# Kernel tuning notes

Measured on AMD Instinct MI355X. Metric: run time of the kernel, lower is better.

The kernel has to match this reference:

```python
import jax, jax.numpy as jnp
import numpy as np

B, C, H, W = 4, 64, 128, 128

def conv1x1(x, w, b):
    # x: [B,Ci,H,W], w: [Co,Ci], b: [Co]
    return jnp.einsum('bchw,oc->bohw', x, w) + b[None, :, None, None]

def setup_inputs() -> dict:
    key = jax.random.key(0)
    ks = jax.random.split(key, 10)
    d = {}
    d['x'] = jax.random.normal(ks[0], (B, C, H, W), dtype=jnp.float32)
    # patchmerging params: LayerNorm(4C) + Linear(4C -> C)
    d['pm_gamma'] = jnp.ones((4 * C,), jnp.float32)
    d['pm_beta'] = jnp.zeros((4 * C,), jnp.float32)
    d['pm_w'] = jax.random.normal(ks[1], (C, 4 * C), jnp.float32) * 0.02
    d['pm_b'] = jnp.zeros((C,), jnp.float32)
    # 1x1 convs: conv2..conv6 are C->C, conv1 is 2C->C
    for i, n in enumerate(['2', '3', '4', '5', '6']):
        d['w' + n] = jax.random.normal(ks[2 + i], (C, C), jnp.float32) * 0.05
        d['b' + n] = jnp.zeros((C,), jnp.float32)
    d['w1'] = jax.random.normal(ks[7], (C, 2 * C), jnp.float32) * 0.05
    d['b1'] = jnp.zeros((C,), jnp.float32)
    return d

def reference(x, pm_gamma, pm_beta, pm_w, pm_b,
              w1, b1, w2, b2, w3, b3, w4, b4, w5, b5, w6, b6):
    Bx, Cx, Hx, Wx = x.shape
    Hh, Wh = Hx // 2, Wx // 2
    N = Hh * Wh
    # ---- patch merging ----
    x0 = x[:, :, 0::2, 0::2]
    x1_ = x[:, :, 1::2, 0::2]
    x2_ = x[:, :, 0::2, 1::2]
    x3_ = x[:, :, 1::2, 1::2]
    m = jnp.concatenate([x0, x1_, x2_, x3_], axis=1)        # [B,4C,Hh,Wh]
    t = m.reshape(Bx, 4 * Cx, N).transpose(0, 2, 1)          # [B,N,4C]
    mu = t.mean(-1, keepdims=True)
    var = t.var(-1, keepdims=True)
    t = (t - mu) / jnp.sqrt(var + 1e-5) * pm_gamma + pm_beta  # LayerNorm eps=1e-5
    t = t @ pm_w.T + pm_b                                     # [B,N,C]
    c1 = t.transpose(0, 2, 1).reshape(Bx, Cx, Hh, Wh)
    # ---- spatial attention (PAM-style) ----
    q = conv1x1(c1, w2, b2).reshape(Bx, Cx, N)
    k = conv1x1(c1, w3, b3).reshape(Bx, Cx, N)
    v = conv1x1(c1, w4, b4).reshape(Bx, Cx, N)
    qk1 = jax.nn.softmax(jnp.einsum('bcn,bcm->bnm', q, k), axis=-1)  # [B,N,N]
    # torch: out1 = v @ qk1.permute(0,2,1) -> out1[b,c,j] = sum_i v[b,c,i]*qk1[b,j,i]
    out1 = jnp.einsum('bci,bji->bcj', v, qk1).reshape(Bx, Cx, Hh, Wh)
    # ---- channel attention (CAM-style) ----
    q2 = conv1x1(c1, w5, b5).reshape(Bx, Cx, N)
    k2 = conv1x1(c1, w6, b6).reshape(Bx, Cx, N)
    qk2 = jax.nn.softmax(jnp.einsum('bcn,bdn->bcd', q2, k2), axis=-1)  # [B,C,C]
    out2 = jnp.einsum('bcd,bdn->bcn', qk2, v).reshape(Bx, Cx, Hh, Wh)
    # ---- fuse, 1x1 conv, bilinear upsample x2 (align_corners=False), residual ----
    out = jnp.concatenate([out1, out2], axis=1)              # [B,2C,Hh,Wh]
    out = conv1x1(out, w1, b1)                               # [B,C,Hh,Wh]
    out = jax.image.resize(out, (Bx, Cx, Hx, Wx), method='bilinear')
    return out + x
```

## Files before the change

kernel.cpp:

```cpp
#include <hip/hip_runtime.h>

typedef __attribute__((ext_vector_type(8))) short bf16x8;
typedef __attribute__((ext_vector_type(4))) float fx4;

struct __attribute__((aligned(8))) sh4 { short x, y, z, w; };

#define OPART_B   0u
#define LSUM_B    12582912u
#define SMALL_B   12976128u
#define L2M_B     17170432u
#define C1B_B     17235968u
#define QB_B      19333120u
#define KB_B      21430272u
#define VCN_B     23527424u
#define VNC_B     25624576u
#define Q2B_B     27721728u
#define K2B_B     29818880u

static __device__ __forceinline__ short f2bf(float f) {
  unsigned u = __float_as_uint(f);
  unsigned r = (u + 0x7FFFu + ((u >> 16) & 1u)) >> 16;
  return (short)r;
}
static __device__ __forceinline__ short f2bf_fast(float f) {
  return (short)((__float_as_uint(f) + 0x8000u) >> 16);
}
static __device__ __forceinline__ float bf2f(short s) {
  return __uint_as_float(((unsigned)(unsigned short)s) << 16);
}
static __device__ __forceinline__ bf16x8 ld8f(const float* p) {
  float4 p0 = *(const float4*)p;
  float4 p1 = *(const float4*)(p + 4);
  bf16x8 r;
  r[0] = f2bf(p0.x); r[1] = f2bf(p0.y); r[2] = f2bf(p0.z); r[3] = f2bf(p0.w);
  r[4] = f2bf(p1.x); r[5] = f2bf(p1.y); r[6] = f2bf(p1.z); r[7] = f2bf(p1.w);
  return r;
}

__global__ __launch_bounds__(256) void patchln_kernel(
    const float* __restrict__ x, const float* __restrict__ gamma,
    const float* __restrict__ beta, const float* __restrict__ pm_w,
    const float* __restrict__ pm_b, short* __restrict__ c1b, float* __restrict__ l2m)
{
  __shared__ short tnb[32*264];
  __shared__ float red_s[512];
  __shared__ float mu_s[32], rs_s[32];
  const int b   = blockIdx.y;
  const int i   = blockIdx.x >> 1;
  const int jh  = blockIdx.x & 1;
  const int tid = threadIdx.x;
  const int j   = tid & 31;
  const int g8  = tid >> 5;
  const int jj  = jh*32 + j;

  if (blockIdx.x == 0) {
    #pragma unroll
    for (int k = 0; k < 16; ++k) l2m[(size_t)b*4096 + k*256 + tid] = 0.0f;
  }

  float vals[32];
  float sm = 0.f, sq = 0.f;
  #pragma unroll
  for (int k = 0; k < 16; ++k) {
    int p  = g8*16 + k;
    int cc = p & 63, di = p >> 6;
    float2 v2 = *(const float2*)&x[((size_t)(b*64 + cc)*128 + 2*i + di)*128 + 2*jj];
    vals[2*k]   = v2.x;
    vals[2*k+1] = v2.y;
    sm += v2.x + v2.y; sq += v2.x*v2.x + v2.y*v2.y;
  }
  red_s[g8*32 + j] = sm;
  red_s[256 + g8*32 + j] = sq;
  __syncthreads();
  if (tid < 32) {
    float s0 = 0.f, q0 = 0.f;
    #pragma unroll
    for (int g = 0; g < 8; ++g) { s0 += red_s[g*32 + tid]; q0 += red_s[256 + g*32 + tid]; }
    float mu  = s0 * (1.0f/256.0f);
    float var = q0 * (1.0f/256.0f) - mu*mu;
    mu_s[tid] = mu;
    rs_s[tid] = rsqrtf(var + 1e-5f);
  }
  __syncthreads();
  {
    float mu = mu_s[j], rs = rs_s[j];
    #pragma unroll
    for (int k = 0; k < 16; ++k) {
      int p  = g8*16 + k;
      int ca = p, cb = p + 128;
      tnb[j*264 + ca] = f2bf((vals[2*k]   - mu)*rs*gamma[ca] + beta[ca]);
      tnb[j*264 + cb] = f2bf((vals[2*k+1] - mu)*rs*gamma[cb] + beta[cb]);
    }
  }
  __syncthreads();

  const int w    = tid >> 6;
  const int lane = tid & 63;
  const int L15  = lane & 15;
  const int quad = lane >> 4;
  fx4 d0 = {0.f,0.f,0.f,0.f}, d1 = {0.f,0.f,0.f,0.f};
  #pragma unroll
  for (int kc = 0; kc < 8; ++kc) {
    bf16x8 a = ld8f(pm_w + (w*16 + L15)*256 + kc*32 + quad*8);
    bf16x8 bf0 = *(const bf16x8*)&tnb[(L15)*264      + kc*32 + quad*8];
    bf16x8 bf1 = *(const bf16x8*)&tnb[(16 + L15)*264 + kc*32 + quad*8];
    d0 = __builtin_amdgcn_mfma_f32_16x16x32_bf16(a, bf0, d0, 0, 0, 0);
    d1 = __builtin_amdgcn_mfma_f32_16x16x32_bf16(a, bf1, d1, 0, 0, 0);
  }
  const int obase = w*16 + quad*4;
  float bias0 = pm_b[obase], bias1 = pm_b[obase+1], bias2 = pm_b[obase+2], bias3 = pm_b[obase+3];
  const int gn0 = i*64 + jh*32 + L15;
  sh4 s0; s0.x = f2bf(d0[0]+bias0); s0.y = f2bf(d0[1]+bias1); s0.z = f2bf(d0[2]+bias2); s0.w = f2bf(d0[3]+bias3);
  sh4 s1; s1.x = f2bf(d1[0]+bias0); s1.y = f2bf(d1[1]+bias1); s1.z = f2bf(d1[2]+bias2); s1.w = f2bf(d1[3]+bias3);
  *(sh4*)&c1b[((size_t)b*4096 + gn0)*64 + obase]      = s0;
  *(sh4*)&c1b[((size_t)b*4096 + gn0 + 16)*64 + obase] = s1;
}

__global__ __launch_bounds__(256) void proj5_kernel(
    const short* __restrict__ c1b,
    const float* __restrict__ w2f, const float* __restrict__ w3f, const float* __restrict__ w4f,
    const float* __restrict__ w5f, const float* __restrict__ w6f,
    const float* __restrict__ b2, const float* __restrict__ b3, const float* __restrict__ b4,
    const float* __restrict__ b5, const float* __restrict__ b6,
    short* __restrict__ qb, short* __restrict__ kb,
    short* __restrict__ vcn, short* __restrict__ vnc,
    short* __restrict__ q2b, short* __restrict__ k2b)
{
  __shared__ short ldsT[4*16*72];
  const int b    = blockIdx.y;
  const int tid  = threadIdx.x;
  const int w    = tid >> 6;
  const int nsub = w & 1;
  const int pg   = w >> 1;
  const int lane = tid & 63;
  const int L15  = lane & 15;
  const int quad = lane >> 4;
  const int gn0  = blockIdx.x*32 + nsub*16;
  const int gn   = gn0 + L15;
  short* T = ldsT + w*16*72;

  bf16x8 bf0 = *(const bf16x8*)&c1b[((size_t)b*4096 + gn)*64 + quad*8];
  bf16x8 bf1 = *(const bf16x8*)&c1b[((size_t)b*4096 + gn)*64 + quad*8 + 32];

  if (pg == 0) {
    const float* wp[2] = {w2f, w3f};
    const float* bp[2] = {b2, b3};
    #pragma unroll
    for (int p = 0; p < 2; ++p) {
      short* dst = (p == 0) ? qb : kb;
      #pragma unroll
      for (int mt = 0; mt < 4; ++mt) {
        bf16x8 a0 = ld8f(wp[p] + (mt*16 + L15)*64 + quad*8);
        bf16x8 a1 = ld8f(wp[p] + (mt*16 + L15)*64 + quad*8 + 32);
        fx4 d = {0.f,0.f,0.f,0.f};
        d = __builtin_amdgcn_mfma_f32_16x16x32_bf16(a0, bf0, d, 0, 0, 0);
        d = __builtin_amdgcn_mfma_f32_16x16x32_bf16(a1, bf1, d, 0, 0, 0);
        const int ob = mt*16 + quad*4;
        sh4 s; s.x = f2bf(d[0]+bp[p][ob]); s.y = f2bf(d[1]+bp[p][ob+1]);
        s.z = f2bf(d[2]+bp[p][ob+2]); s.w = f2bf(d[3]+bp[p][ob+3]);
        *(sh4*)&dst[((size_t)b*4096 + gn)*64 + ob] = s;
      }
    }
    #pragma unroll
    for (int mt = 0; mt < 4; ++mt) {
      bf16x8 a0 = ld8f(w4f + (mt*16 + L15)*64 + quad*8);
      bf16x8 a1 = ld8f(w4f + (mt*16 + L15)*64 + quad*8 + 32);
      fx4 d = {0.f,0.f,0.f,0.f};
      d = __builtin_amdgcn_mfma_f32_16x16x32_bf16(a0, bf0, d, 0, 0, 0);
      d = __builtin_amdgcn_mfma_f32_16x16x32_bf16(a1, bf1, d, 0, 0, 0);
      const int ob = mt*16 + quad*4;
      sh4 s; s.x = f2bf(d[0]+b4[ob]); s.y = f2bf(d[1]+b4[ob+1]);
      s.z = f2bf(d[2]+b4[ob+2]); s.w = f2bf(d[3]+b4[ob+3]);
      *(sh4*)&vnc[((size_t)b*4096 + gn)*64 + ob] = s;
      *(sh4*)&T[L15*72 + ob] = s;
    }
    {
      const int o = lane;
      bf16x8 r0, r1;
      #pragma unroll
      for (int n = 0; n < 8; ++n) r0[n] = T[n*72 + o];
      #pragma unroll
      for (int n = 0; n < 8; ++n) r1[n] = T[(n+8)*72 + o];
      *(bf16x8*)&vcn[(size_t)b*262144 + (size_t)o*4096 + gn0]     = r0;
      *(bf16x8*)&vcn[(size_t)b*262144 + (size_t)o*4096 + gn0 + 8] = r1;
    }
  } else {
    const float* wp[2] = {w5f, w6f};
    const float* bp[2] = {b5, b6};
    #pragma unroll
    for (int p = 0; p < 2; ++p) {
      short* dst = (p == 0) ? q2b : k2b;
      #pragma unroll
      for (int mt = 0; mt < 4; ++mt) {
        bf16x8 a0 = ld8f(wp[p] + (mt*16 + L15)*64 + quad*8);
        bf16x8 a1 = ld8f(wp[p] + (mt*16 + L15)*64 + quad*8 + 32);
        fx4 d = {0.f,0.f,0.f,0.f};
        d = __builtin_amdgcn_mfma_f32_16x16x32_bf16(a0, bf0, d, 0, 0, 0);
        d = __builtin_amdgcn_mfma_f32_16x16x32_bf16(a1, bf1, d, 0, 0, 0);
        const int ob = mt*16 + quad*4;
        sh4 s; s.x = f2bf(d[0]+bp[p][ob]); s.y = f2bf(d[1]+bp[p][ob+1]);
        s.z = f2bf(d[2]+bp[p][ob+2]); s.w = f2bf(d[3]+bp[p][ob+3]);
        *(sh4*)&T[L15*72 + ob] = s;
      }
      const int o = lane;
      bf16x8 r0, r1;
      #pragma unroll
      for (int n = 0; n < 8; ++n) r0[n] = T[n*72 + o];
      #pragma unroll
      for (int n = 0; n < 8; ++n) r1[n] = T[(n+8)*72 + o];
      *(bf16x8*)&dst[(size_t)b*262144 + (size_t)o*4096 + gn0]     = r0;
      *(bf16x8*)&dst[(size_t)b*262144 + (size_t)o*4096 + gn0 + 8] = r1;
    }
  }
}

__global__ __launch_bounds__(256) void flash_kernel(
    const short* __restrict__ Qb, const short* __restrict__ Kb,
    const short* __restrict__ Vcn, short* __restrict__ opart, float* __restrict__ lsum,
    const short* __restrict__ q2b, const short* __restrict__ k2b, float* __restrict__ L2M)
{
  __shared__ short lds_s[24576];
  const int b    = blockIdx.z;
  const int s    = blockIdx.y;
  const int tid  = threadIdx.x;
  const int w    = tid >> 6;
  const int lane = tid & 63;
  const int L15  = lane & 15;
  const int quad = lane >> 4;

  if (s == 6) {
    const int n0 = blockIdx.x * 128;
    const short* qg = q2b + (size_t)b*262144;
    const short* kg = k2b + (size_t)b*262144;
    fx4 D[4] = {{0.f,0.f,0.f,0.f},{0.f,0.f,0.f,0.f},{0.f,0.f,0.f,0.f},{0.f,0.f,0.f,0.f}};
    #pragma unroll
    for (int kc = 0; kc < 4; ++kc) {
      bf16x8 a = *(const bf16x8*)&qg[(w*16 + L15)*4096 + n0 + kc*32 + quad*8];
      #pragma unroll
      for (int nt = 0; nt < 4; ++nt) {
        bf16x8 bb = *(const bf16x8*)&kg[(nt*16 + L15)*4096 + n0 + kc*32 + quad*8];
        D[nt] = __builtin_amdgcn_mfma_f32_16x16x32_bf16(a, bb, D[nt], 0, 0, 0);
      }
    }
    float* Lb = L2M + (size_t)b*4096;
    #pragma unroll
    for (int nt = 0; nt < 4; ++nt)
      #pragma unroll
      for (int r = 0; r < 4; ++r)
        atomicAdd(&Lb[(w*16 + quad*4 + r)*64 + nt*16 + L15], D[nt][r]);
    return;
  }

  short* ktb = lds_s;
  short* vsb = lds_s + 8192;
  short* ps  = lds_s + 16384;

  const int q0   = blockIdx.x << 7;
  const int t0   = (s < 4) ? s*11 : 44 + (s - 4)*10;
  const int cnt  = (s < 4) ? 11 : 10;
  const int jbase = w*32;

  const short* Qg = Qb  + (size_t)b*262144;
  const short* Kg = Kb  + (size_t)b*262144;
  const short* Vg = Vcn + (size_t)b*262144;

  bf16x8 qa[2][2];
  #pragma unroll
  for (int jt = 0; jt < 2; ++jt)
    #pragma unroll
    for (int h = 0; h < 2; ++h)
      qa[jt][h] = *(const bf16x8*)(Qg + (size_t)(q0 + jbase + jt*16 + L15)*64 + h*32 + quad*8);

  bf16x8 ones;
  #pragma unroll
  for (int u = 0; u < 8; ++u) ones[u] = (short)0x3F80;

  const int si  = tid >> 2;
  const int scb = (tid & 3) * 2;
  const int s0k = scb ^ (si & 7);
  const int s1k = s0k ^ 1;

  {
    const int i0 = t0 << 6;
    bf16x8 kr0 = *(const bf16x8*)(Kg + (size_t)(i0 + si)*64 + scb*8);
    bf16x8 kr1 = *(const bf16x8*)(Kg + (size_t)(i0 + si)*64 + scb*8 + 8);
    bf16x8 vr0 = *(const bf16x8*)(Vg + (size_t)si*4096 + i0 + (tid&3)*16);
    bf16x8 vr1 = *(const bf16x8*)(Vg + (size_t)si*4096 + i0 + (tid&3)*16 + 8);
    *(bf16x8*)(ktb + si*64 + s0k*8) = kr0;
    *(bf16x8*)(ktb + si*64 + s1k*8) = kr1;
    *(bf16x8*)(vsb + si*64 + s0k*8) = vr0;
    *(bf16x8*)(vsb + si*64 + s1k*8) = vr1;
  }
  __syncthreads();

  fx4 oacc[2][4];
  #pragma unroll
  for (int jt = 0; jt < 2; ++jt)
    #pragma unroll
    for (int ct = 0; ct < 4; ++ct) oacc[jt][ct] = (fx4){0.f,0.f,0.f,0.f};
  fx4 lacc[2] = {{0.f,0.f,0.f,0.f},{0.f,0.f,0.f,0.f}};

  const int cbx0 = quad       ^ (L15 & 7);
  const int cbx1 = (quad + 4) ^ (L15 & 7);
  const int jk   = L15 & 7;
  const int pu   = (quad >> 1);
  const int ph   = (quad & 1) << 2;

  for (int t = 0; t < cnt; ++t) {
    const short* kt = ktb + (t & 1)*4096;
    const short* vv = vsb + (t & 1)*4096;
    short* ktn = ktb + ((t + 1) & 1)*4096;
    short* vsn = vsb + ((t + 1) & 1)*4096;

    bf16x8 kr0, kr1, vr0, vr1;
    const bool pf = (t < cnt - 1);
    if (pf) {
      const int i0n = (t0 + t + 1) << 6;
      kr0 = *(const bf16x8*)(Kg + (size_t)(i0n + si)*64 + scb*8);
      kr1 = *(const bf16x8*)(Kg + (size_t)(i0n + si)*64 + scb*8 + 8);
      vr0 = *(const bf16x8*)(Vg + (size_t)si*4096 + i0n + (tid&3)*16);
      vr1 = *(const bf16x8*)(Vg + (size_t)si*4096 + i0n + (tid&3)*16 + 8);
    }

    fx4 d2[4][2];
    #pragma unroll
    for (int mt = 0; mt < 4; ++mt)
      #pragma unroll
      for (int jt = 0; jt < 2; ++jt) d2[mt][jt] = (fx4){0.f,0.f,0.f,0.f};
    #pragma unroll
    for (int mt = 0; mt < 4; ++mt) {
      bf16x8 ak0 = *(const bf16x8*)(kt + (mt*16 + L15)*64 + cbx0*8);
      bf16x8 ak1 = *(const bf16x8*)(kt + (mt*16 + L15)*64 + cbx1*8);
      d2[mt][0] = __builtin_amdgcn_mfma_f32_16x16x32_bf16(ak0, qa[0][0], d2[mt][0], 0, 0, 0);
      d2[mt][1] = __builtin_amdgcn_mfma_f32_16x16x32_bf16(ak0, qa[1][0], d2[mt][1], 0, 0, 0);
      d2[mt][0] = __builtin_amdgcn_mfma_f32_16x16x32_bf16(ak1, qa[0][1], d2[mt][0], 0, 0, 0);
      d2[mt][1] = __builtin_amdgcn_mfma_f32_16x16x32_bf16(ak1, qa[1][1], d2[mt][1], 0, 0, 0);
    }

    #pragma unroll
    for (int mt = 0; mt < 4; ++mt) {
      const int slot0 = ((mt*2 + pu) ^ jk) << 3;
      #pragma unroll
      for (int jt = 0; jt < 2; ++jt) {
        const int j = jbase + jt*16 + L15;
        sh4 pv;
        pv.x = f2bf_fast(__expf(d2[mt][jt][0]));
        pv.y = f2bf_fast(__expf(d2[mt][jt][1]));
        pv.z = f2bf_fast(__expf(d2[mt][jt][2]));
        pv.w = f2bf_fast(__expf(d2[mt][jt][3]));
        *(sh4*)&ps[j*64 + slot0 + ph] = pv;
      }
    }

    bf16x8 pb[2][2];
    #pragma unroll
    for (int jt = 0; jt < 2; ++jt) {
      const int jrow = jbase + jt*16 + L15;
      pb[jt][0] = *(const bf16x8*)&ps[jrow*64 + (((quad    ) ^ jk) << 3)];
      pb[jt][1] = *(const bf16x8*)&ps[jrow*64 + (((quad + 4) ^ jk) << 3)];
    }

    #pragma unroll
    for (int jt = 0; jt < 2; ++jt) {
      lacc[jt] = __builtin_amdgcn_mfma_f32_16x16x32_bf16(ones, pb[jt][0], lacc[jt], 0, 0, 0);
      lacc[jt] = __builtin_amdgcn_mfma_f32_16x16x32_bf16(ones, pb[jt][1], lacc[jt], 0, 0, 0);
    }

    #pragma unroll
    for (int ct = 0; ct < 4; ++ct) {
      bf16x8 va0 = *(const bf16x8*)(vv + (ct*16 + L15)*64 + cbx0*8);
      bf16x8 va1 = *(const bf16x8*)(vv + (ct*16 + L15)*64 + cbx1*8);
      #pragma unroll
      for (int jt = 0; jt < 2; ++jt) {
        oacc[jt][ct] = __builtin_amdgcn_mfma_f32_16x16x32_bf16(va0, pb[jt][0], oacc[jt][ct], 0, 0, 0);
        oacc[jt][ct] = __builtin_amdgcn_mfma_f32_16x16x32_bf16(va1, pb[jt][1], oacc[jt][ct], 0, 0, 0);
      }
    }

    if (pf) {
      *(bf16x8*)(ktn + si*64 + s0k*8) = kr0;
      *(bf16x8*)(ktn + si*64 + s1k*8) = kr1;
      *(bf16x8*)(vsn + si*64 + s0k*8) = vr0;
      *(bf16x8*)(vsn + si*64 + s1k*8) = vr1;
    }
    __syncthreads();
  }

  const size_t srow = ((size_t)(b*6 + s)*4096) + q0;
  #pragma unroll
  for (int jt = 0; jt < 2; ++jt) {
    const size_t nrow = srow + jbase + jt*16 + L15;
    #pragma unroll
    for (int ct = 0; ct < 4; ++ct) {
      sh4 sv;
      sv.x = f2bf(oacc[jt][ct][0]); sv.y = f2bf(oacc[jt][ct][1]);
      sv.z = f2bf(oacc[jt][ct][2]); sv.w = f2bf(oacc[jt][ct][3]);
      *(sh4*)&opart[nrow*64 + ct*16 + quad*4] = sv;
    }
    if (quad == 0) lsum[nrow] = lacc[jt][0];
  }
}

__global__ __launch_bounds__(256) void tail_kernel(
    const short* __restrict__ opart, const float* __restrict__ lsum,
    const float* __restrict__ l2m, const short* __restrict__ vnc,
    const float* __restrict__ w1f, const float* __restrict__ b1,
    float* __restrict__ sml)
{
  __shared__ short p2[4096];
  __shared__ short cat[4096];
  const int b    = blockIdx.y;
  const int n0   = blockIdx.x << 5;
  const int tid  = threadIdx.x;
  const int w    = tid >> 6;
  const int lane = tid & 63;
  const int L15  = lane & 15;
  const int quad = lane >> 4;

  if (tid < 64) {
    const float* Lr = l2m + (size_t)b*4096 + tid*64;
    float vrow[64];
    float mx = -1e30f;
    #pragma unroll
    for (int d4 = 0; d4 < 16; ++d4) {
      float4 v4 = *(const float4*)&Lr[d4*4];
      vrow[d4*4+0] = v4.x; vrow[d4*4+1] = v4.y; vrow[d4*4+2] = v4.z; vrow[d4*4+3] = v4.w;
      mx = fmaxf(mx, fmaxf(fmaxf(v4.x, v4.y), fmaxf(v4.z, v4.w)));
    }
    float sme = 0.f;
    #pragma unroll
    for (int d = 0; d < 64; ++d) { vrow[d] = __expf(vrow[d] - mx); sme += vrow[d]; }
    const float inv = 1.0f / sme;
    const int key = tid & 7;
    #pragma unroll
    for (int g = 0; g < 8; ++g) {
      bf16x8 pk;
      #pragma unroll
      for (int u = 0; u < 8; ++u) pk[u] = f2bf(vrow[g*8 + u] * inv);
      *(bf16x8*)&p2[tid*64 + ((g ^ key) << 3)] = pk;
    }
  }

  {
    const int nl = tid >> 3;
    const int c0 = (tid & 7) << 3;
    const int n  = n0 + nl;
    float l = 0.f;
    #pragma unroll
    for (int sp = 0; sp < 6; ++sp) l += lsum[((size_t)(b*6 + sp)*4096) + n];
    const float inv = 1.0f / l;
    float acc[8];
    #pragma unroll
    for (int u = 0; u < 8; ++u) acc[u] = 0.f;
    #pragma unroll
    for (int sp = 0; sp < 6; ++sp) {
      bf16x8 A0 = *(const bf16x8*)&opart[(((size_t)(b*6 + sp)*4096) + n)*64 + c0];
      #pragma unroll
      for (int u = 0; u < 8; ++u) acc[u] += bf2f(A0[u]);
    }
    const int key = nl & 7;
    const int g = (c0 >> 3) ^ key;
    bf16x8 s0;
    #pragma unroll
    for (int u = 0; u < 8; ++u) s0[u] = f2bf(acc[u]*inv);
    *(bf16x8*)&cat[nl*128 + (g << 3)] = s0;
  }
  __syncthreads();

  {
    const int nl  = (w & 1)*16 + L15;
    const int n   = n0 + nl;
    const int mh  = w >> 1;
    const int key = L15 & 7;
    bf16x8 vb0 = *(const bf16x8*)&vnc[((size_t)b*4096 + n)*64 + quad*8];
    bf16x8 vb1 = *(const bf16x8*)&vnc[((size_t)b*4096 + n)*64 + quad*8 + 32];
    #pragma unroll
    for (int mi = 0; mi < 2; ++mi) {
      const int mt = mh*2 + mi;
      bf16x8 a0 = *(const bf16x8*)&p2[(mt*16 + L15)*64 + (((quad    ) ^ key) << 3)];
      bf16x8 a1 = *(const bf16x8*)&p2[(mt*16 + L15)*64 + (((quad + 4) ^ key) << 3)];
      fx4 d = {0.f,0.f,0.f,0.f};
      d = __builtin_amdgcn_mfma_f32_16x16x32_bf16(a0, vb0, d, 0, 0, 0);
      d = __builtin_amdgcn_mfma_f32_16x16x32_bf16(a1, vb1, d, 0, 0, 0);
      const int c = 64 + mt*16 + quad*4;
      const int g = (c >> 3) ^ key;
      sh4 sv; sv.x = f2bf(d[0]); sv.y = f2bf(d[1]); sv.z = f2bf(d[2]); sv.w = f2bf(d[3]);
      *(sh4*)&cat[nl*128 + (g << 3) + (quad & 1)*4] = sv;
    }
  }
  __syncthreads();

  {
    const int nl  = (w & 1)*16 + L15;
    const int mh  = w >> 1;
    const int key = L15 & 7;
    bf16x8 bfr[4];
    #pragma unroll
    for (int kc = 0; kc < 4; ++kc) {
      const int g = (kc*4 + quad) ^ key;
      bfr[kc] = *(const bf16x8*)&cat[nl*128 + (g << 3)];
    }
    #pragma unroll
    for (int mi = 0; mi < 2; ++mi) {
      const int mt = mh*2 + mi;
      fx4 d = {0.f,0.f,0.f,0.f};
      #pragma unroll
      for (int kc = 0; kc < 4; ++kc) {
        bf16x8 a = ld8f(w1f + (mt*16 + L15)*128 + kc*32 + quad*8);
        d = __builtin_amdgcn_mfma_f32_16x16x32_bf16(a, bfr[kc], d, 0, 0, 0);
      }
      const int ob = mt*16 + quad*4;
      #pragma unroll
      for (int r = 0; r < 4; ++r)
        sml[((size_t)b*64 + ob + r)*4096 + n0 + nl] = d[r] + b1[ob + r];
    }
  }
}

__global__ __launch_bounds__(256) void upsample_kernel(
    const float* __restrict__ sml, const float* __restrict__ x, float* __restrict__ out)
{
  int idx = blockIdx.x*256 + threadIdx.x;
  int jp = idx & 63;
  int I  = (idx >> 6) & 127;
  int bo = idx >> 13;
  int ih = I >> 1;
  int i0, i1; float wi0, wi1;
  if (I & 1) { i0 = ih;                 i1 = (ih < 63) ? ih+1 : 63; wi0 = 0.75f; wi1 = 0.25f; }
  else       { i0 = (ih > 0) ? ih-1 : 0; i1 = ih;                   wi0 = 0.25f; wi1 = 0.75f; }
  const int jm = (jp > 0)  ? jp-1 : 0;
  const int jx = (jp < 63) ? jp+1 : 63;
  const float* sp = sml + (size_t)bo*4096;
  float a0 = sp[i0*64 + jm], a1 = sp[i0*64 + jp], a2 = sp[i0*64 + jx];
  float b0 = sp[i1*64 + jm], b1v = sp[i1*64 + jp], b2v = sp[i1*64 + jx];
  float re0 = wi0*(0.25f*a0 + 0.75f*a1) + wi1*(0.25f*b0 + 0.75f*b1v);
  float re1 = wi0*(0.75f*a1 + 0.25f*a2) + wi1*(0.75f*b1v + 0.25f*b2v);
  const size_t obase = ((size_t)bo*128 + I)*128 + jp*2;
  float2 xr = *(const float2*)&x[obase];
  *(float2*)&out[obase] = make_float2(re0 + xr.x, re1 + xr.y);
}

extern "C" void kernel_launch(void* const* d_in, const int* in_sizes, int n_in,
                              void* d_out, int out_size, void* d_ws, size_t ws_size,
                              hipStream_t stream) {
  const float* x     = (const float*)d_in[0];
  const float* gamma = (const float*)d_in[1];
  const float* beta  = (const float*)d_in[2];
  const float* pm_w  = (const float*)d_in[3];
  const float* pm_b  = (const float*)d_in[4];
  const float* w2 = (const float*)d_in[5];  const float* b2 = (const float*)d_in[6];
  const float* w3 = (const float*)d_in[7];  const float* b3 = (const float*)d_in[8];
  const float* w4 = (const float*)d_in[9];  const float* b4 = (const float*)d_in[10];
  const float* w5 = (const float*)d_in[11]; const float* b5 = (const float*)d_in[12];
  const float* w6 = (const float*)d_in[13]; const float* b6 = (const float*)d_in[14];
  const float* w1 = (const float*)d_in[15]; const float* b1 = (const float*)d_in[16];
  char* wsb  = (char*)d_ws;
  float* out = (float*)d_out;

  short* opart = (short*)(wsb + OPART_B);
  float* lsum  = (float*)(wsb + LSUM_B);
  float* sml   = (float*)(wsb + SMALL_B);
  float* l2m   = (float*)(wsb + L2M_B);
  short* c1b   = (short*)(wsb + C1B_B);
  short* qb    = (short*)(wsb + QB_B);
  short* kb    = (short*)(wsb + KB_B);
  short* vcn   = (short*)(wsb + VCN_B);
  short* vnc   = (short*)(wsb + VNC_B);
  short* q2b   = (short*)(wsb + Q2B_B);
  short* k2b   = (short*)(wsb + K2B_B);

  patchln_kernel<<<dim3(128,4), dim3(256), 0, stream>>>(x, gamma, beta, pm_w, pm_b, c1b, l2m);
  proj5_kernel<<<dim3(128,4), dim3(256), 0, stream>>>(c1b, w2, w3, w4, w5, w6,
      b2, b3, b4, b5, b6, qb, kb, vcn, vnc, q2b, k2b);
  flash_kernel<<<dim3(32,7,4), dim3(256), 0, stream>>>(qb, kb, vcn, opart, lsum, q2b, k2b, l2m);
  tail_kernel<<<dim3(128,4), dim3(256), 0, stream>>>(opart, lsum, l2m, vnc, w1, b1, sml);
  upsample_kernel<<<dim3(8192), dim3(256), 0, stream>>>(sml, x, out);
}
```

Before: 163.1 us.

## Fuse patch-merge LayerNorm with Q/K/V projections and pre-convert weights to bf16

The patch-merge LayerNorm+linear kernel is merged with the five 1x1 projection kernel. The intermediate c1 tile now stays in swizzled LDS instead of making a round trip through global memory. A new small prep kernel converts all weight matrices to bf16 once per call and zeroes the l2m accumulator. The projection and tail MFMA loops then load bf16 weights directly instead of converting fp32 in every block. This adds one extra launch and uses more LDS per block in the fused kernel.

```diff
diff --git a/kernel.cpp b/kernel.cpp
--- a/kernel.cpp
+++ b/kernel.cpp
@@ -9,13 +9,19 @@
 #define LSUM_B    12582912u
 #define SMALL_B   12976128u
 #define L2M_B     17170432u
-#define C1B_B     17235968u
-#define QB_B      19333120u
-#define KB_B      21430272u
-#define VCN_B     23527424u
-#define VNC_B     25624576u
-#define Q2B_B     27721728u
-#define K2B_B     29818880u
+#define PMB_B     17235968u
+#define W2B_B     17268736u
+#define W3B_B     17276928u
+#define W4B_B     17285120u
+#define W5B_B     17293312u
+#define W6B_B     17301504u
+#define W1B_B     17309696u
+#define QB_B      17326080u
+#define KB_B      19423232u
+#define VCN_B     21520384u
+#define VNC_B     23617536u
+#define Q2B_B     25714688u
+#define K2B_B     27811840u
 
 static __device__ __forceinline__ short f2bf(float f) {
   unsigned u = __float_as_uint(f);
@@ -28,21 +34,41 @@
 static __device__ __forceinline__ float bf2f(short s) {
   return __uint_as_float(((unsigned)(unsigned short)s) << 16);
 }
-static __device__ __forceinline__ bf16x8 ld8f(const float* p) {
-  float4 p0 = *(const float4*)p;
-  float4 p1 = *(const float4*)(p + 4);
-  bf16x8 r;
-  r[0] = f2bf(p0.x); r[1] = f2bf(p0.y); r[2] = f2bf(p0.z); r[3] = f2bf(p0.w);
-  r[4] = f2bf(p1.x); r[5] = f2bf(p1.y); r[6] = f2bf(p1.z); r[7] = f2bf(p1.w);
-  return r;
-}
-
-__global__ __launch_bounds__(256) void patchln_kernel(
+
+__global__ __launch_bounds__(256) void prep_kernel(
+    const float* __restrict__ pm_w, const float* __restrict__ w2,
+    const float* __restrict__ w3,  const float* __restrict__ w4,
+    const float* __restrict__ w5,  const float* __restrict__ w6,
+    const float* __restrict__ w1,  char* __restrict__ wsb)
+{
+  int tid = blockIdx.x * 256 + threadIdx.x;
+  ((short*)(wsb + PMB_B))[tid] = f2bf(pm_w[tid]);
+  if (tid < 4096) {
+    ((short*)(wsb + W2B_B))[tid] = f2bf(w2[tid]);
+    ((short*)(wsb + W3B_B))[tid] = f2bf(w3[tid]);
+    ((short*)(wsb + W4B_B))[tid] = f2bf(w4[tid]);
+    ((short*)(wsb + W5B_B))[tid] = f2bf(w5[tid]);
+    ((short*)(wsb + W6B_B))[tid] = f2bf(w6[tid]);
+  }
+  if (tid < 8192) ((short*)(wsb + W1B_B))[tid] = f2bf(w1[tid]);
+  ((float*)(wsb + L2M_B))[tid] = 0.0f;
+}
+
+__global__ __launch_bounds__(256) void patchproj_kernel(
     const float* __restrict__ x, const float* __restrict__ gamma,
-    const float* __restrict__ beta, const float* __restrict__ pm_w,
-    const float* __restrict__ pm_b, short* __restrict__ c1b, float* __restrict__ l2m)
+    const float* __restrict__ beta, const short* __restrict__ pmb,
+    const float* __restrict__ pm_b,
+    const short* __restrict__ w2b, const short* __restrict__ w3b, const short* __restrict__ w4b,
+    const short* __restrict__ w5b, const short* __restrict__ w6b,
+    const float* __restrict__ b2, const float* __restrict__ b3, const float* __restrict__ b4,
+    const float* __restrict__ b5, const float* __restrict__ b6,
+    short* __restrict__ qb, short* __restrict__ kb,
+    short* __restrict__ vcn, short* __restrict__ vnc,
+    short* __restrict__ q2b, short* __restrict__ k2b)
 {
   __shared__ short tnb[32*264];
+  __shared__ short c1t[32*64];
+  __shared__ short ldsT[4*16*72];
   __shared__ float red_s[512];
   __shared__ float mu_s[32], rs_s[32];
   const int b   = blockIdx.y;
@@ -52,11 +78,6 @@
   const int j   = tid & 31;
   const int g8  = tid >> 5;
   const int jj  = jh*32 + j;
-
-  if (blockIdx.x == 0) {
-    #pragma unroll
-    for (int k = 0; k < 16; ++k) l2m[(size_t)b*4096 + k*256 + tid] = 0.0f;
-  }
 
   float vals[32];
   float sm = 0.f, sq = 0.f;
@@ -98,60 +119,49 @@
   const int lane = tid & 63;
   const int L15  = lane & 15;
   const int quad = lane >> 4;
-  fx4 d0 = {0.f,0.f,0.f,0.f}, d1 = {0.f,0.f,0.f,0.f};
-  #pragma unroll
-  for (int kc = 0; kc < 8; ++kc) {
-    bf16x8 a = ld8f(pm_w + (w*16 + L15)*256 + kc*32 + quad*8);
-    bf16x8 bf0 = *(const bf16x8*)&tnb[(L15)*264      + kc*32 + quad*8];
-    bf16x8 bf1 = *(const bf16x8*)&tnb[(16 + L15)*264 + kc*32 + quad*8];
-    d0 = __builtin_amdgcn_mfma_f32_16x16x32_bf16(a, bf0, d0, 0, 0, 0);
-    d1 = __builtin_amdgcn_mfma_f32_16x16x32_bf16(a, bf1, d1, 0, 0, 0);
-  }
-  const int obase = w*16 + quad*4;
-  float bias0 = pm_b[obase], bias1 = pm_b[obase+1], bias2 = pm_b[obase+2], bias3 = pm_b[obase+3];
-  const int gn0 = i*64 + jh*32 + L15;
-  sh4 s0; s0.x = f2bf(d0[0]+bias0); s0.y = f2bf(d0[1]+bias1); s0.z = f2bf(d0[2]+bias2); s0.w = f2bf(d0[3]+bias3);
-  sh4 s1; s1.x = f2bf(d1[0]+bias0); s1.y = f2bf(d1[1]+bias1); s1.z = f2bf(d1[2]+bias2); s1.w = f2bf(d1[3]+bias3);
-  *(sh4*)&c1b[((size_t)b*4096 + gn0)*64 + obase]      = s0;
-  *(sh4*)&c1b[((size_t)b*4096 + gn0 + 16)*64 + obase] = s1;
-}
-
-__global__ __launch_bounds__(256) void proj5_kernel(
-    const short* __restrict__ c1b,
-    const float* __restrict__ w2f, const float* __restrict__ w3f, const float* __restrict__ w4f,
-    const float* __restrict__ w5f, const float* __restrict__ w6f,
-    const float* __restrict__ b2, const float* __restrict__ b3, const float* __restrict__ b4,
-    const float* __restrict__ b5, const float* __restrict__ b6,
-    short* __restrict__ qb, short* __restrict__ kb,
-    short* __restrict__ vcn, short* __restrict__ vnc,
-    short* __restrict__ q2b, short* __restrict__ k2b)
-{
-  __shared__ short ldsT[4*16*72];
-  const int b    = blockIdx.y;
-  const int tid  = threadIdx.x;
-  const int w    = tid >> 6;
+  {
+    fx4 d0 = {0.f,0.f,0.f,0.f}, d1 = {0.f,0.f,0.f,0.f};
+    #pragma unroll
+    for (int kc = 0; kc < 8; ++kc) {
+      bf16x8 a  = *(const bf16x8*)&pmb[(w*16 + L15)*256 + kc*32 + quad*8];
+      bf16x8 bf0 = *(const bf16x8*)&tnb[(L15)*264      + kc*32 + quad*8];
+      bf16x8 bf1 = *(const bf16x8*)&tnb[(16 + L15)*264 + kc*32 + quad*8];
+      d0 = __builtin_amdgcn_mfma_f32_16x16x32_bf16(a, bf0, d0, 0, 0, 0);
+      d1 = __builtin_amdgcn_mfma_f32_16x16x32_bf16(a, bf1, d1, 0, 0, 0);
+    }
+    const int obase = w*16 + quad*4;
+    float bias0 = pm_b[obase], bias1 = pm_b[obase+1], bias2 = pm_b[obase+2], bias3 = pm_b[obase+3];
+    const int gq  = (obase >> 3);
+    const int hh  = (quad & 1) * 4;
+    const int key = L15 & 7;
+    sh4 s0; s0.x = f2bf(d0[0]+bias0); s0.y = f2bf(d0[1]+bias1); s0.z = f2bf(d0[2]+bias2); s0.w = f2bf(d0[3]+bias3);
+    sh4 s1; s1.x = f2bf(d1[0]+bias0); s1.y = f2bf(d1[1]+bias1); s1.z = f2bf(d1[2]+bias2); s1.w = f2bf(d1[3]+bias3);
+    *(sh4*)&c1t[(L15)*64      + ((gq ^ key) << 3) + hh] = s0;
+    *(sh4*)&c1t[(16 + L15)*64 + ((gq ^ key) << 3) + hh] = s1;
+  }
+  __syncthreads();
+
   const int nsub = w & 1;
   const int pg   = w >> 1;
-  const int lane = tid & 63;
-  const int L15  = lane & 15;
-  const int quad = lane >> 4;
-  const int gn0  = blockIdx.x*32 + nsub*16;
+  const int gn0  = i*64 + jh*32 + nsub*16;
   const int gn   = gn0 + L15;
+  const int nl   = nsub*16 + L15;
+  const int key  = L15 & 7;
   short* T = ldsT + w*16*72;
 
-  bf16x8 bf0 = *(const bf16x8*)&c1b[((size_t)b*4096 + gn)*64 + quad*8];
-  bf16x8 bf1 = *(const bf16x8*)&c1b[((size_t)b*4096 + gn)*64 + quad*8 + 32];
+  bf16x8 bf0 = *(const bf16x8*)&c1t[nl*64 + (((quad    ) ^ key) << 3)];
+  bf16x8 bf1 = *(const bf16x8*)&c1t[nl*64 + (((quad + 4) ^ key) << 3)];
 
   if (pg == 0) {
-    const float* wp[2] = {w2f, w3f};
+    const short* wp[2] = {w2b, w3b};
     const float* bp[2] = {b2, b3};
     #pragma unroll
     for (int p = 0; p < 2; ++p) {
       short* dst = (p == 0) ? qb : kb;
       #pragma unroll
       for (int mt = 0; mt < 4; ++mt) {
-        bf16x8 a0 = ld8f(wp[p] + (mt*16 + L15)*64 + quad*8);
-        bf16x8 a1 = ld8f(wp[p] + (mt*16 + L15)*64 + quad*8 + 32);
+        bf16x8 a0 = *(const bf16x8*)&wp[p][(mt*16 + L15)*64 + quad*8];
+        bf16x8 a1 = *(const bf16x8*)&wp[p][(mt*16 + L15)*64 + quad*8 + 32];
         fx4 d = {0.f,0.f,0.f,0.f};
         d = __builtin_amdgcn_mfma_f32_16x16x32_bf16(a0, bf0, d, 0, 0, 0);
         d = __builtin_amdgcn_mfma_f32_16x16x32_bf16(a1, bf1, d, 0, 0, 0);
@@ -163,8 +173,8 @@
     }
     #pragma unroll
     for (int mt = 0; mt < 4; ++mt) {
-      bf16x8 a0 = ld8f(w4f + (mt*16 + L15)*64 + quad*8);
-      bf16x8 a1 = ld8f(w4f + (mt*16 + L15)*64 + quad*8 + 32);
+      bf16x8 a0 = *(const bf16x8*)&w4b[(mt*16 + L15)*64 + quad*8];
+      bf16x8 a1 = *(const bf16x8*)&w4b[(mt*16 + L15)*64 + quad*8 + 32];
       fx4 d = {0.f,0.f,0.f,0.f};
       d = __builtin_amdgcn_mfma_f32_16x16x32_bf16(a0, bf0, d, 0, 0, 0);
       d = __builtin_amdgcn_mfma_f32_16x16x32_bf16(a1, bf1, d, 0, 0, 0);
@@ -185,15 +195,15 @@
       *(bf16x8*)&vcn[(size_t)b*262144 + (size_t)o*4096 + gn0 + 8] = r1;
     }
   } else {
-    const float* wp[2] = {w5f, w6f};
+    const short* wp[2] = {w5b, w6b};
     const float* bp[2] = {b5, b6};
     #pragma unroll
     for (int p = 0; p < 2; ++p) {
       short* dst = (p == 0) ? q2b : k2b;
       #pragma unroll
       for (int mt = 0; mt < 4; ++mt) {
-        bf16x8 a0 = ld8f(wp[p] + (mt*16 + L15)*64 + quad*8);
-        bf16x8 a1 = ld8f(wp[p] + (mt*16 + L15)*64 + quad*8 + 32);
+        bf16x8 a0 = *(const bf16x8*)&wp[p][(mt*16 + L15)*64 + quad*8];
+        bf16x8 a1 = *(const bf16x8*)&wp[p][(mt*16 + L15)*64 + quad*8 + 32];
         fx4 d = {0.f,0.f,0.f,0.f};
         d = __builtin_amdgcn_mfma_f32_16x16x32_bf16(a0, bf0, d, 0, 0, 0);
         d = __builtin_amdgcn_mfma_f32_16x16x32_bf16(a1, bf1, d, 0, 0, 0);
@@ -404,7 +414,7 @@
 __global__ __launch_bounds__(256) void tail_kernel(
     const short* __restrict__ opart, const float* __restrict__ lsum,
     const float* __restrict__ l2m, const short* __restrict__ vnc,
-    const float* __restrict__ w1f, const float* __restrict__ b1,
+    const short* __restrict__ w1b, const float* __restrict__ b1,
     float* __restrict__ sml)
 {
   __shared__ short p2[4096];
@@ -506,7 +516,7 @@
       fx4 d = {0.f,0.f,0.f,0.f};
       #pragma unroll
       for (int kc = 0; kc < 4; ++kc) {
-        bf16x8 a = ld8f(w1f + (mt*16 + L15)*128 + kc*32 + quad*8);
+        bf16x8 a = *(const bf16x8*)&w1b[(mt*16 + L15)*128 + kc*32 + quad*8];
         d = __builtin_amdgcn_mfma_f32_16x16x32_bf16(a, bfr[kc], d, 0, 0, 0);
       }
       const int ob = mt*16 + quad*4;
@@ -561,7 +571,13 @@
   float* lsum  = (float*)(wsb + LSUM_B);
   float* sml   = (float*)(wsb + SMALL_B);
   float* l2m   = (float*)(wsb + L2M_B);
-  short* c1b   = (short*)(wsb + C1B_B);
+  short* pmb   = (short*)(wsb + PMB_B);
+  short* w2b   = (short*)(wsb + W2B_B);
+  short* w3b   = (short*)(wsb + W3B_B);
+  short* w4b   = (short*)(wsb + W4B_B);
+  short* w5b   = (short*)(wsb + W5B_B);
+  short* w6b   = (short*)(wsb + W6B_B);
+  short* w1b   = (short*)(wsb + W1B_B);
   short* qb    = (short*)(wsb + QB_B);
   short* kb    = (short*)(wsb + KB_B);
   short* vcn   = (short*)(wsb + VCN_B);
@@ -569,10 +585,10 @@
   short* q2b   = (short*)(wsb + Q2B_B);
   short* k2b   = (short*)(wsb + K2B_B);
 
-  patchln_kernel<<<dim3(128,4), dim3(256), 0, stream>>>(x, gamma, beta, pm_w, pm_b, c1b, l2m);
-  proj5_kernel<<<dim3(128,4), dim3(256), 0, stream>>>(c1b, w2, w3, w4, w5, w6,
-      b2, b3, b4, b5, b6, qb, kb, vcn, vnc, q2b, k2b);
+  prep_kernel<<<dim3(64), dim3(256), 0, stream>>>(pm_w, w2, w3, w4, w5, w6, w1, wsb);
+  patchproj_kernel<<<dim3(128,4), dim3(256), 0, stream>>>(x, gamma, beta, pmb, pm_b,
+      w2b, w3b, w4b, w5b, w6b, b2, b3, b4, b5, b6, qb, kb, vcn, vnc, q2b, k2b);
   flash_kernel<<<dim3(32,7,4), dim3(256), 0, stream>>>(qb, kb, vcn, opart, lsum, q2b, k2b, l2m);
-  tail_kernel<<<dim3(128,4), dim3(256), 0, stream>>>(opart, lsum, l2m, vnc, w1, b1, sml);
+  tail_kernel<<<dim3(128,4), dim3(256), 0, stream>>>(opart, lsum, l2m, vnc, w1b, b1, sml);
   upsample_kernel<<<dim3(8192), dim3(256), 0, stream>>>(sml, x, out);
 }
```

Result: faster. 152.9 us (-6.3%).
